# Kernel tuning notes

Hardware: AMD Instinct MI355X
Metric: run time of the kernel (lower is better)

## Reference

```python
import jax, jax.numpy as jnp
import numpy as np

N, DIN, DOUT = 8192, 512, 256


def setup_inputs() -> dict:
    key = jax.random.key(0)
    ks = jax.random.split(key, 8)
    s_in = 1.0 / np.sqrt(DIN)   # ~ torch Linear default init scale
    s_out = 1.0 / np.sqrt(DOUT)
    return {
        "x": jax.random.normal(ks[0], (N, DIN), jnp.float32),
        "Wm": jax.random.normal(ks[1], (DIN, DOUT), jnp.float32) * s_in,
        "Wn": jax.random.normal(ks[2], (DIN, DOUT), jnp.float32) * s_in,
        "Wr": jax.random.normal(ks[3], (DIN, DOUT), jnp.float32) * s_in,
        "Wt": jax.random.normal(ks[4], (DIN, DOUT), jnp.float32) * s_in,
        "Wrg": jax.random.normal(ks[5], (DOUT, DOUT), jnp.float32) * s_out,
        "brg": jnp.zeros((DOUT,), jnp.float32),
        "Wlg": jax.random.normal(ks[6], (DOUT, DOUT), jnp.float32) * s_out,
        "blg": jnp.zeros((DOUT,), jnp.float32),
        "Wp": jax.random.normal(ks[7], (DOUT, 1), jnp.float32) * s_out,
        "bp": jnp.zeros((1,), jnp.float32),
    }


def reference(x, Wm, Wn, Wr, Wt, Wrg, brg, Wlg, blg, Wp, bp):
    n = x.shape[0]
    xm = x @ Wm                      # [N, 256]
    xn = x @ Wn                      # [N, 256]
    # pairwise Euclidean distance via GEMM trick (avoids O(N^2*D) diff tensor)
    sq = (jnp.sum(xm * xm, axis=-1)[:, None]
          + jnp.sum(xn * xn, axis=-1)[None, :]
          - 2.0 * (xm @ xn.T))       # [N, N]
    dist = jnp.sqrt(jnp.maximum(sq, 0.0)) * 0.5
    exps = jnp.exp(-dist) / (n / 64.0)
    eye = jnp.eye(n, dtype=x.dtype)
    adj = exps * (1.0 - eye) + eye   # unit diagonal, scaled off-diagonal
    xr = adj @ (x @ Wr)              # graph conv: [N,N]@[N,256]
    xl = x @ Wt
    w = jax.nn.sigmoid(xr @ Wrg + brg + xl @ Wlg + blg)
    feat = (1.0 - w) * xr + w * xl   # gated fusion
    score = feat @ Wp + bp           # [N, 1]
    return adj, score
```

## Files before the change

kernel.cpp:

```cpp
#include <hip/hip_runtime.h>
#include <stdint.h>

typedef __attribute__((ext_vector_type(8))) short bf16x8;
typedef __attribute__((ext_vector_type(4))) float f32x4;
typedef __attribute__((ext_vector_type(4))) unsigned int u32x4;

__device__ __forceinline__ unsigned short f2bf(float f){
  unsigned u = __float_as_uint(f);
  u += 0x7FFFu + ((u >> 16) & 1u);
  return (unsigned short)(u >> 16);
}
__device__ __forceinline__ float bf2f(unsigned short s){
  return __uint_as_float(((unsigned)s) << 16);
}

__device__ __forceinline__ int lds_off(int r, int b){
  return r * 128 + (b ^ ((r & 7) << 4));
}
__device__ __forceinline__ int ldsP_off(int r, int b){
  return r * 256 + (b ^ ((r & 7) << 4));
}

__device__ __forceinline__ void cp16(const unsigned short* g, unsigned short* l){
  __builtin_amdgcn_global_load_lds(
      (const __attribute__((address_space(1))) unsigned int*)g,
      (__attribute__((address_space(3))) unsigned int*)l, 16, 0, 0);
}

template<int ROWS, int NT>
__device__ __forceinline__ void stage_async(unsigned short* lds, const unsigned short* g,
                                            long row0, long stride, long k0, int tid){
#pragma unroll
  for (int c = tid; c < ROWS * 8; c += NT){
    int r = c >> 3, s = c & 7;
    int ss = s ^ (r & 7);
    cp16(g + (row0 + r) * stride + k0 + ss * 8, lds + (long)(c & ~63) * 8);
  }
}

__device__ __forceinline__ int xcd_swz(int bid, int nwg){
  int q = nwg >> 3;
  return (bid & 7) * q + (bid >> 3);
}

__global__ __launch_bounds__(256) void k_prep(const float* x, const float* Wm, const float* Wn,
    const float* Wr, const float* Wt, const float* Wrg, const float* Wlg, const float* bp,
    unsigned short* WT, unsigned short* WcatT, unsigned short* xbf, float* nm, float* nn,
    float* score){
  long id = (long)blockIdx.x * 256 + threadIdx.x;
  if (id < 1024L * 512){
    int n = (int)(id >> 9), k = (int)(id & 511);
    const float* W = (n < 256) ? Wm : ((n < 512) ? Wn : ((n < 768) ? Wr : Wt));
    WT[id] = f2bf(W[(long)k * 256 + (n & 255)]);
  }
  if (id < 256L * 512){
    int n = (int)(id >> 9), k = (int)(id & 511);
    WcatT[id] = f2bf(k < 256 ? Wrg[(long)k * 256 + n] : Wlg[(long)(k - 256) * 256 + n]);
  }
  if (id < 8192){ score[id] = bp[0]; nm[id] = 0.f; nn[id] = 0.f; }
  long xe = id * 8;
  float4 v0 = *(const float4*)(x + xe);
  float4 v1 = *(const float4*)(x + xe + 4);
  unsigned short t[8] = { f2bf(v0.x), f2bf(v0.y), f2bf(v0.z), f2bf(v0.w),
                          f2bf(v1.x), f2bf(v1.y), f2bf(v1.z), f2bf(v1.w) };
  *(uint4*)(xbf + xe) = *(const uint4*)t;
}

__global__ __launch_bounds__(256, 3) void k_gemmA(const unsigned short* xbf, const unsigned short* WT,
    unsigned short* xm, unsigned short* xn, unsigned short* xwrT, unsigned short* xl,
    float* nm, float* nn){
  __shared__ unsigned short ldsA[128 * 64];
  __shared__ unsigned short ldsB[128 * 64];
  int tid = threadIdx.x, lane = tid & 63, w = tid >> 6;
  int r = lane & 15, gq = lane >> 4;
  int wi = w >> 1, wc = w & 1;
  int swz = xcd_swz(blockIdx.x, 512);
  int bm = swz & 63, bn = swz >> 6;

  f32x4 acc[4][4];
  f32x4 zero = {0.f, 0.f, 0.f, 0.f};
#pragma unroll
  for (int m = 0; m < 4; ++m)
#pragma unroll
    for (int n = 0; n < 4; ++n) acc[m][n] = zero;

  for (int k0 = 0; k0 < 512; k0 += 64){
    __syncthreads();
    stage_async<128, 256>(ldsA, xbf, (long)bm * 128, 512, k0, tid);
    stage_async<128, 256>(ldsB, WT, (long)bn * 128, 512, k0, tid);
    __syncthreads();
#pragma unroll
    for (int ks = 0; ks < 2; ++ks){
      int bb = ks * 64 + gq * 16;
      bf16x8 a[4], b[4];
#pragma unroll
      for (int m = 0; m < 4; ++m)
        a[m] = *(const bf16x8*)((const char*)ldsA + lds_off(wi * 64 + m * 16 + r, bb));
#pragma unroll
      for (int n = 0; n < 4; ++n)
        b[n] = *(const bf16x8*)((const char*)ldsB + lds_off(wc * 64 + n * 16 + r, bb));
#pragma unroll
      for (int m = 0; m < 4; ++m)
#pragma unroll
        for (int n = 0; n < 4; ++n)
          acc[m][n] = __builtin_amdgcn_mfma_f32_16x16x32_bf16(b[n], a[m], acc[m][n], 0, 0, 0);
    }
  }
#pragma unroll
  for (int m = 0; m < 4; ++m){
    int i = bm * 128 + wi * 64 + m * 16 + r;
#pragma unroll
    for (int n = 0; n < 4; ++n){
      int ng = bn * 128 + wc * 64 + n * 16 + gq * 4;
      int sector = ng >> 8, nc = ng & 255;
      unsigned short p[4] = { f2bf(acc[m][n][0]), f2bf(acc[m][n][1]),
                              f2bf(acc[m][n][2]), f2bf(acc[m][n][3]) };
      if (sector == 2){
#pragma unroll
        for (int q = 0; q < 4; ++q) xwrT[(long)(nc + q) * 8192 + i] = p[q];
      } else {
        unsigned short* dst = sector == 0 ? xm : (sector == 1 ? xn : xl);
        *(uint2*)(dst + (long)i * 256 + nc) = *(const uint2*)p;
      }
    }
    if (bn < 4){
      float s = 0.f;
#pragma unroll
      for (int n = 0; n < 4; ++n)
#pragma unroll
        for (int q = 0; q < 4; ++q) s += acc[m][n][q] * acc[m][n][q];
      s += __shfl_xor(s, 16);
      s += __shfl_xor(s, 32);
      if (gq == 0) atomicAdd(((bn < 2) ? nm : nn) + i, s);
    }
  }
}

__global__ __launch_bounds__(512, 1) void k_fused(
    const unsigned short* xm, const unsigned short* xn,
    const float* nm, const float* nn, const unsigned short* xwrT,
    float* adj, float* partial, int ntiles, int NS){
  __shared__ char smem[131072];
  char* ldsP = smem + 65536;
  unsigned short* ldsW = (unsigned short*)(smem + 98304);

  int tid = threadIdx.x, lane = tid & 63, w = tid >> 6;
  int r = lane & 15, gq = lane >> 4;
  int wi = w >> 2, wj = w & 3;
  int sp = blockIdx.x % NS, bm = blockIdx.x / NS;

  f32x4 zero = {0.f, 0.f, 0.f, 0.f};
  f32x4 acc2[4][4];
#pragma unroll
  for (int m = 0; m < 4; ++m)
#pragma unroll
    for (int n = 0; n < 4; ++n) acc2[m][n] = zero;

  float nmi[4];
#pragma unroll
  for (int m = 0; m < 4; ++m) nmi[m] = nm[bm * 128 + wi * 64 + m * 16 + r];

  long prevColBase = 0;

  for (int t = 0; t < ntiles; ++t){
    int bn = sp * ntiles + t;
    f32x4 acc1[4][2];
#pragma unroll
    for (int m = 0; m < 4; ++m)
#pragma unroll
      for (int n = 0; n < 2; ++n) acc1[m][n] = zero;

    stage_async<128, 512>((unsigned short*)smem, xm, (long)bm * 128, 256, 0, tid);
    stage_async<128, 512>((unsigned short*)(smem + 16384), xn, (long)bn * 128, 256, 0, tid);
    __syncthreads();
#pragma unroll
    for (int kk = 0; kk < 4; ++kk){
      char* cb = smem + (kk & 1) * 32768;
      if (kk < 3){
        char* nb = smem + ((kk + 1) & 1) * 32768;
        stage_async<128, 512>((unsigned short*)nb, xm, (long)bm * 128, 256, (kk + 1) * 64, tid);
        stage_async<128, 512>((unsigned short*)(nb + 16384), xn, (long)bn * 128, 256, (kk + 1) * 64, tid);
      }
      if (t > 0){
        int row = kk * 32 + (tid >> 4), cs = tid & 15;
        uint4 pv = *(const uint4*)(ldsP + ldsP_off(row, cs * 16));
        const unsigned short* pb = (const unsigned short*)&pv;
        long ge = (long)(bm * 128 + row) * 8192 + prevColBase + cs * 8;
        f32x4 v0 = { bf2f(pb[0]), bf2f(pb[1]), bf2f(pb[2]), bf2f(pb[3]) };
        f32x4 v1 = { bf2f(pb[4]), bf2f(pb[5]), bf2f(pb[6]), bf2f(pb[7]) };
        __builtin_nontemporal_store(v0, (f32x4*)(adj + ge));
        __builtin_nontemporal_store(v1, (f32x4*)(adj + ge + 4));
      }
      unsigned short* ldsA = (unsigned short*)cb;
      unsigned short* ldsB = (unsigned short*)(cb + 16384);
      __builtin_amdgcn_s_setprio(1);
#pragma unroll
      for (int ks = 0; ks < 2; ++ks){
        int bb = ks * 64 + gq * 16;
        bf16x8 a[4], b[2];
#pragma unroll
        for (int m = 0; m < 4; ++m)
          a[m] = *(const bf16x8*)((const char*)ldsA + lds_off(wi * 64 + m * 16 + r, bb));
#pragma unroll
        for (int n = 0; n < 2; ++n)
          b[n] = *(const bf16x8*)((const char*)ldsB + lds_off(wj * 32 + n * 16 + r, bb));
#pragma unroll
        for (int m = 0; m < 4; ++m)
#pragma unroll
          for (int n = 0; n < 2; ++n)
            acc1[m][n] = __builtin_amdgcn_mfma_f32_16x16x32_bf16(b[n], a[m], acc1[m][n], 0, 0, 0);
      }
      __builtin_amdgcn_s_setprio(0);
      __syncthreads();
    }

#pragma unroll
    for (int n = 0; n < 2; ++n){
      int jl0 = wj * 32 + n * 16 + gq * 4;
      int jb = bn * 128 + jl0;
      float4 nn4 = *(const float4*)(nn + jb);
      const float nnq[4] = { nn4.x, nn4.y, nn4.z, nn4.w };
#pragma unroll
      for (int m = 0; m < 4; ++m){
        int il = wi * 64 + m * 16 + r;
        int i = bm * 128 + il;
        unsigned short pv[4];
#pragma unroll
        for (int q = 0; q < 4; ++q){
          float sq = nmi[m] + nnq[q] - 2.f * acc1[m][n][q];
          float d = sqrtf(fmaxf(sq, 0.f)) * 0.5f;
          float v = (i == jb + q) ? 1.f : __expf(-d) * (1.f / 128.f);
          pv[q] = f2bf(v);
        }
        *(uint2*)(ldsP + ldsP_off(il, jl0 * 2)) = *(const uint2*)pv;
      }
    }
    __syncthreads();

#pragma unroll
    for (int kh = 0; kh < 2; ++kh){
      stage_async<256, 512>(ldsW, xwrT, 0, 8192, (long)bn * 128 + kh * 64, tid);
      __syncthreads();
      __builtin_amdgcn_s_setprio(1);
#pragma unroll
      for (int ks = 0; ks < 2; ++ks){
        bf16x8 a[4], b[4];
#pragma unroll
        for (int m = 0; m < 4; ++m)
          a[m] = *(const bf16x8*)(ldsP + ldsP_off(wi * 64 + m * 16 + r, kh * 128 + ks * 64 + gq * 16));
#pragma unroll
        for (int n = 0; n < 4; ++n)
          b[n] = *(const bf16x8*)((const char*)ldsW + lds_off(wj * 64 + n * 16 + r, ks * 64 + gq * 16));
#pragma unroll
        for (int m = 0; m < 4; ++m)
#pragma unroll
          for (int n = 0; n < 4; ++n)
            acc2[m][n] = __builtin_amdgcn_mfma_f32_16x16x32_bf16(b[n], a[m], acc2[m][n], 0, 0, 0);
      }
      __builtin_amdgcn_s_setprio(0);
      __syncthreads();
    }
    prevColBase = (long)bn * 128;
  }

#pragma unroll
  for (int o = 0; o < 4; ++o){
    int c = o * 512 + tid;
    int row = c >> 4, cs = c & 15;
    uint4 pv = *(const uint4*)(ldsP + ldsP_off(row, cs * 16));
    const unsigned short* pb = (const unsigned short*)&pv;
    long ge = (long)(bm * 128 + row) * 8192 + prevColBase + cs * 8;
    f32x4 v0 = { bf2f(pb[0]), bf2f(pb[1]), bf2f(pb[2]), bf2f(pb[3]) };
    f32x4 v1 = { bf2f(pb[4]), bf2f(pb[5]), bf2f(pb[6]), bf2f(pb[7]) };
    __builtin_nontemporal_store(v0, (f32x4*)(adj + ge));
    __builtin_nontemporal_store(v1, (f32x4*)(adj + ge + 4));
  }

  float* dst = partial + (long)sp * 8192 * 256;
#pragma unroll
  for (int m = 0; m < 4; ++m){
    int i = bm * 128 + wi * 64 + m * 16 + r;
#pragma unroll
    for (int n = 0; n < 4; ++n){
      int cb = wj * 64 + n * 16 + gq * 4;
      __builtin_nontemporal_store(acc2[m][n], (f32x4*)(dst + (long)i * 256 + cb));
    }
  }
}

__global__ __launch_bounds__(512, 2) void k_gate(const float* partial, int S,
    const unsigned short* xl, const unsigned short* WcatT,
    const float* brg, const float* blg, const float* Wp, float* score){
  __shared__ unsigned short ldsA[128 * 64];
  __shared__ unsigned short ldsB[256 * 64];
  int tid = threadIdx.x, lane = tid & 63, w = tid >> 6;
  int r = lane & 15, gq = lane >> 4;
  int wi = w >> 2, wc = w & 3;
  int bm = blockIdx.x;

  f32x4 acc[4][4];
  f32x4 zero = {0.f, 0.f, 0.f, 0.f};
#pragma unroll
  for (int m = 0; m < 4; ++m)
#pragma unroll
    for (int n = 0; n < 4; ++n) acc[m][n] = zero;

  uint2 xrf[4][4], xlf[4][4];

  for (int t = 0; t < 8; ++t){
    __syncthreads();
    if (t < 4){
#pragma unroll
      for (int u = 0; u < 2; ++u){
        int c = tid + u * 512;
        int rr = c >> 3, s = c & 7;
        long gi = (long)(bm * 128 + rr) * 256 + t * 64 + s * 8;
        f32x4 a0 = __builtin_nontemporal_load((const f32x4*)(partial + gi));
        f32x4 a1 = __builtin_nontemporal_load((const f32x4*)(partial + gi + 4));
        for (int sp = 1; sp < S; ++sp){
          long go = (long)sp * 8192 * 256 + gi;
          a0 += __builtin_nontemporal_load((const f32x4*)(partial + go));
          a1 += __builtin_nontemporal_load((const f32x4*)(partial + go + 4));
        }
        unsigned short tb[8] = { f2bf(a0[0]), f2bf(a0[1]), f2bf(a0[2]), f2bf(a0[3]),
                                 f2bf(a1[0]), f2bf(a1[1]), f2bf(a1[2]), f2bf(a1[3]) };
        *(uint4*)((char*)ldsA + lds_off(rr, s * 16)) = *(const uint4*)tb;
      }
    } else {
      stage_async<128, 512>(ldsA, xl, (long)bm * 128, 256, (t - 4) * 64, tid);
    }
    stage_async<256, 512>(ldsB, WcatT, 0, 512, (long)t * 64, tid);
    __syncthreads();

    if (t == wc || t == wc + 4){
#pragma unroll
      for (int m = 0; m < 4; ++m){
        int il = wi * 64 + m * 16 + r;
#pragma unroll
        for (int n = 0; n < 4; ++n){
          uint2 v = *(const uint2*)((const char*)ldsA + lds_off(il, (n * 16 + gq * 4) * 2));
          if (t < 4) xrf[m][n] = v; else xlf[m][n] = v;
        }
      }
    }
#pragma unroll
    for (int ks = 0; ks < 2; ++ks){
      int bb = ks * 64 + gq * 16;
      bf16x8 a[4], b[4];
#pragma unroll
      for (int m = 0; m < 4; ++m)
        a[m] = *(const bf16x8*)((const char*)ldsA + lds_off(wi * 64 + m * 16 + r, bb));
#pragma unroll
      for (int n = 0; n < 4; ++n)
        b[n] = *(const bf16x8*)((const char*)ldsB + lds_off(wc * 64 + n * 16 + r, bb));
#pragma unroll
      for (int m = 0; m < 4; ++m)
#pragma unroll
        for (int n = 0; n < 4; ++n)
          acc[m][n] = __builtin_amdgcn_mfma_f32_16x16x32_bf16(b[n], a[m], acc[m][n], 0, 0, 0);
    }
  }

#pragma unroll
  for (int m = 0; m < 4; ++m){
    int i = bm * 128 + wi * 64 + m * 16 + r;
    float part = 0.f;
#pragma unroll
    for (int n = 0; n < 4; ++n){
      int cb = wc * 64 + n * 16 + gq * 4;
      float4 b4  = *(const float4*)(brg + cb);
      float4 l4  = *(const float4*)(blg + cb);
      float4 wp4 = *(const float4*)(Wp + cb);
      const unsigned short* xr4 = (const unsigned short*)&xrf[m][n];
      const unsigned short* xl4 = (const unsigned short*)&xlf[m][n];
      const float bq[4] = { b4.x, b4.y, b4.z, b4.w };
      const float lq[4] = { l4.x, l4.y, l4.z, l4.w };
      const float pq[4] = { wp4.x, wp4.y, wp4.z, wp4.w };
#pragma unroll
      for (int q = 0; q < 4; ++q){
        float arg = acc[m][n][q] + bq[q] + lq[q];
        float wv = 1.f / (1.f + __expf(-arg));
        float feat = (1.f - wv) * bf2f(xr4[q]) + wv * bf2f(xl4[q]);
        part += feat * pq[q];
      }
    }
    part += __shfl_xor(part, 16);
    part += __shfl_xor(part, 32);
    if (gq == 0) atomicAdd(score + i, part);
  }
}

extern "C" void kernel_launch(void* const* d_in, const int* in_sizes, int n_in,
                              void* d_out, int out_size, void* d_ws, size_t ws_size,
                              hipStream_t stream){
  const float* x   = (const float*)d_in[0];
  const float* Wm  = (const float*)d_in[1];
  const float* Wn  = (const float*)d_in[2];
  const float* Wr  = (const float*)d_in[3];
  const float* Wt  = (const float*)d_in[4];
  const float* Wrg = (const float*)d_in[5];
  const float* brg = (const float*)d_in[6];
  const float* Wlg = (const float*)d_in[7];
  const float* blg = (const float*)d_in[8];
  const float* Wp  = (const float*)d_in[9];
  const float* bp  = (const float*)d_in[10];

  float* adj   = (float*)d_out;
  float* score = adj + 8192L * 8192;

  char* wsb = (char*)d_ws;
  unsigned short* xm    = (unsigned short*)(wsb);
  unsigned short* xn    = (unsigned short*)(wsb + (4L  << 20));
  unsigned short* xwrT  = (unsigned short*)(wsb + (8L  << 20));
  unsigned short* xl    = (unsigned short*)(wsb + (12L << 20));
  float*          nm    = (float*)         (wsb + (20L << 20));
  float*          nn    = nm + 8192;
  unsigned short* WT    = (unsigned short*)(wsb + (21L << 20));
  unsigned short* WcatT = (unsigned short*)(wsb + (22L << 20));
  unsigned short* xbf   = (unsigned short*)(wsb + (23L << 20));
  float*          partial = (float*)(wsb + (31L << 20));

  size_t base = 31L << 20;
  int NS = 1;
  if      (ws_size >= base + 8 * (8L << 20)) NS = 8;
  else if (ws_size >= base + 4 * (8L << 20)) NS = 4;
  else if (ws_size >= base + 2 * (8L << 20)) NS = 2;

  k_prep  <<<2048, 256, 0, stream>>>(x, Wm, Wn, Wr, Wt, Wrg, Wlg, bp, WT, WcatT, xbf, nm, nn, score);
  k_gemmA <<<512, 256, 0, stream>>>(xbf, WT, xm, xn, xwrT, xl, nm, nn);
  k_fused <<<64 * NS, 512, 0, stream>>>(xm, xn, nm, nn, xwrT, adj, partial, 64 / NS, NS);
  k_gate  <<<64, 512, 0, stream>>>(partial, NS, xl, WcatT, brg, blg, Wp, score);
}
```

Baseline: 287.9 us.

## Defer adj@xwr GEMM to next tile, load xwr directly, shrink LDS for occupancy

The fused distance/adjacency kernel now runs the second GEMM (P tile times xwr) one tile late and overlaps it with the next tile's first-GEMM staging. The xwr operand is read straight from global memory into registers, with no LDS staging. The first GEMM uses a K-step of 32 with a smaller double buffer, so LDS per block drops from 128KB to 64KB and launch bounds allow more resident blocks. In exchange, the uncoalesced global reads of xwr rely on L2, the first GEMM needs more barriers, and register pressure may rise under the higher launch-bounds target.

```diff
diff --git a/kernel.cpp b/kernel.cpp
--- a/kernel.cpp
+++ b/kernel.cpp
@@ -17,6 +17,9 @@
 __device__ __forceinline__ int lds_off(int r, int b){
   return r * 128 + (b ^ ((r & 7) << 4));
 }
+__device__ __forceinline__ int lds32_off(int r, int b){
+  return r * 64 + (b ^ ((r & 3) << 4));
+}
 __device__ __forceinline__ int ldsP_off(int r, int b){
   return r * 256 + (b ^ ((r & 7) << 4));
 }
@@ -38,9 +41,11 @@
   }
 }
 
-__device__ __forceinline__ int xcd_swz(int bid, int nwg){
-  int q = nwg >> 3;
-  return (bid & 7) * q + (bid >> 3);
+__device__ __forceinline__ void stage32(unsigned short* lds, const unsigned short* g,
+                                        long row0, long stride, long k0, int tid){
+  int r = tid >> 2, s = tid & 3;
+  int ss = s ^ (r & 3);
+  cp16(g + (row0 + r) * stride + k0 + ss * 8, lds + (long)(tid & ~63) * 8);
 }
 
 __global__ __launch_bounds__(256) void k_prep(const float* x, const float* Wm, const float* Wn,
@@ -74,7 +79,8 @@
   int tid = threadIdx.x, lane = tid & 63, w = tid >> 6;
   int r = lane & 15, gq = lane >> 4;
   int wi = w >> 1, wc = w & 1;
-  int swz = xcd_swz(blockIdx.x, 512);
+  int q8 = 512 >> 3;
+  int swz = (blockIdx.x & 7) * q8 + (blockIdx.x >> 3);
   int bm = swz & 63, bn = swz >> 6;
 
   f32x4 acc[4][4];
@@ -136,13 +142,12 @@
   }
 }
 
-__global__ __launch_bounds__(512, 1) void k_fused(
+__global__ __launch_bounds__(512, 4) void k_fused(
     const unsigned short* xm, const unsigned short* xn,
     const float* nm, const float* nn, const unsigned short* xwrT,
     float* adj, float* partial, int ntiles, int NS){
-  __shared__ char smem[131072];
-  char* ldsP = smem + 65536;
-  unsigned short* ldsW = (unsigned short*)(smem + 98304);
+  __shared__ char smem[65536];
+  char* ldsP = smem + 32768;
 
   int tid = threadIdx.x, lane = tid & 63, w = tid >> 6;
   int r = lane & 15, gq = lane >> 4;
@@ -160,56 +165,78 @@
 #pragma unroll
   for (int m = 0; m < 4; ++m) nmi[m] = nm[bm * 128 + wi * 64 + m * 16 + r];
 
-  long prevColBase = 0;
+  long prevCol = 0;
 
   for (int t = 0; t < ntiles; ++t){
     int bn = sp * ntiles + t;
-    f32x4 acc1[4][2];
-#pragma unroll
-    for (int m = 0; m < 4; ++m)
-#pragma unroll
-      for (int n = 0; n < 2; ++n) acc1[m][n] = zero;
-
-    stage_async<128, 512>((unsigned short*)smem, xm, (long)bm * 128, 256, 0, tid);
-    stage_async<128, 512>((unsigned short*)(smem + 16384), xn, (long)bn * 128, 256, 0, tid);
-    __syncthreads();
-#pragma unroll
-    for (int kk = 0; kk < 4; ++kk){
-      char* cb = smem + (kk & 1) * 32768;
-      if (kk < 3){
-        char* nb = smem + ((kk + 1) & 1) * 32768;
-        stage_async<128, 512>((unsigned short*)nb, xm, (long)bm * 128, 256, (kk + 1) * 64, tid);
-        stage_async<128, 512>((unsigned short*)(nb + 16384), xn, (long)bn * 128, 256, (kk + 1) * 64, tid);
-      }
-      if (t > 0){
-        int row = kk * 32 + (tid >> 4), cs = tid & 15;
+
+    stage32((unsigned short*)smem, xm, (long)bm * 128, 256, 0, tid);
+    stage32((unsigned short*)(smem + 8192), xn, (long)bn * 128, 256, 0, tid);
+
+    if (t > 0){
+#pragma unroll
+      for (int o = 0; o < 4; ++o){
+        int c = o * 512 + tid;
+        int row = c >> 4, cs = c & 15;
         uint4 pv = *(const uint4*)(ldsP + ldsP_off(row, cs * 16));
         const unsigned short* pb = (const unsigned short*)&pv;
-        long ge = (long)(bm * 128 + row) * 8192 + prevColBase + cs * 8;
+        long ge = (long)(bm * 128 + row) * 8192 + prevCol + cs * 8;
         f32x4 v0 = { bf2f(pb[0]), bf2f(pb[1]), bf2f(pb[2]), bf2f(pb[3]) };
         f32x4 v1 = { bf2f(pb[4]), bf2f(pb[5]), bf2f(pb[6]), bf2f(pb[7]) };
         __builtin_nontemporal_store(v0, (f32x4*)(adj + ge));
         __builtin_nontemporal_store(v1, (f32x4*)(adj + ge + 4));
       }
+#pragma unroll
+      for (int ks = 0; ks < 4; ++ks){
+        bf16x8 a[4], b[4];
+#pragma unroll
+        for (int n = 0; n < 4; ++n){
+          long c = wj * 64 + n * 16 + r;
+          b[n] = *(const bf16x8*)(xwrT + c * 8192 + prevCol + ks * 32 + gq * 8);
+        }
+#pragma unroll
+        for (int m = 0; m < 4; ++m)
+          a[m] = *(const bf16x8*)(ldsP + ldsP_off(wi * 64 + m * 16 + r, ks * 64 + gq * 16));
+        __builtin_amdgcn_s_setprio(1);
+#pragma unroll
+        for (int m = 0; m < 4; ++m)
+#pragma unroll
+          for (int n = 0; n < 4; ++n)
+            acc2[m][n] = __builtin_amdgcn_mfma_f32_16x16x32_bf16(b[n], a[m], acc2[m][n], 0, 0, 0);
+        __builtin_amdgcn_s_setprio(0);
+      }
+    }
+    __syncthreads();
+
+    f32x4 acc1[4][2];
+#pragma unroll
+    for (int m = 0; m < 4; ++m)
+#pragma unroll
+      for (int n = 0; n < 2; ++n) acc1[m][n] = zero;
+
+#pragma unroll
+    for (int kk = 0; kk < 8; ++kk){
+      char* cb = smem + (kk & 1) * 16384;
+      if (kk < 7){
+        char* nb = smem + ((kk + 1) & 1) * 16384;
+        stage32((unsigned short*)nb, xm, (long)bm * 128, 256, (kk + 1) * 32, tid);
+        stage32((unsigned short*)(nb + 8192), xn, (long)bn * 128, 256, (kk + 1) * 32, tid);
+      }
       unsigned short* ldsA = (unsigned short*)cb;
-      unsigned short* ldsB = (unsigned short*)(cb + 16384);
+      unsigned short* ldsB = (unsigned short*)(cb + 8192);
+      bf16x8 a[4], b[2];
+#pragma unroll
+      for (int m = 0; m < 4; ++m)
+        a[m] = *(const bf16x8*)((const char*)ldsA + lds32_off(wi * 64 + m * 16 + r, gq * 16));
+#pragma unroll
+      for (int n = 0; n < 2; ++n)
+        b[n] = *(const bf16x8*)((const char*)ldsB + lds32_off(wj * 32 + n * 16 + r, gq * 16));
       __builtin_amdgcn_s_setprio(1);
 #pragma unroll
-      for (int ks = 0; ks < 2; ++ks){
-        int bb = ks * 64 + gq * 16;
-        bf16x8 a[4], b[2];
-#pragma unroll
-        for (int m = 0; m < 4; ++m)
-          a[m] = *(const bf16x8*)((const char*)ldsA + lds_off(wi * 64 + m * 16 + r, bb));
+      for (int m = 0; m < 4; ++m)
 #pragma unroll
         for (int n = 0; n < 2; ++n)
-          b[n] = *(const bf16x8*)((const char*)ldsB + lds_off(wj * 32 + n * 16 + r, bb));
-#pragma unroll
-        for (int m = 0; m < 4; ++m)
-#pragma unroll
-          for (int n = 0; n < 2; ++n)
-            acc1[m][n] = __builtin_amdgcn_mfma_f32_16x16x32_bf16(b[n], a[m], acc1[m][n], 0, 0, 0);
-      }
+          acc1[m][n] = __builtin_amdgcn_mfma_f32_16x16x32_bf16(b[n], a[m], acc1[m][n], 0, 0, 0);
       __builtin_amdgcn_s_setprio(0);
       __syncthreads();
     }
@@ -235,33 +262,10 @@
         *(uint2*)(ldsP + ldsP_off(il, jl0 * 2)) = *(const uint2*)pv;
       }
     }
-    __syncthreads();
-
-#pragma unroll
-    for (int kh = 0; kh < 2; ++kh){
-      stage_async<256, 512>(ldsW, xwrT, 0, 8192, (long)bn * 128 + kh * 64, tid);
-      __syncthreads();
-      __builtin_amdgcn_s_setprio(1);
-#pragma unroll
-      for (int ks = 0; ks < 2; ++ks){
-        bf16x8 a[4], b[4];
-#pragma unroll
-        for (int m = 0; m < 4; ++m)
-          a[m] = *(const bf16x8*)(ldsP + ldsP_off(wi * 64 + m * 16 + r, kh * 128 + ks * 64 + gq * 16));
-#pragma unroll
-        for (int n = 0; n < 4; ++n)
-          b[n] = *(const bf16x8*)((const char*)ldsW + lds_off(wj * 64 + n * 16 + r, ks * 64 + gq * 16));
-#pragma unroll
-        for (int m = 0; m < 4; ++m)
-#pragma unroll
-          for (int n = 0; n < 4; ++n)
-            acc2[m][n] = __builtin_amdgcn_mfma_f32_16x16x32_bf16(b[n], a[m], acc2[m][n], 0, 0, 0);
-      }
-      __builtin_amdgcn_s_setprio(0);
-      __syncthreads();
-    }
-    prevColBase = (long)bn * 128;
-  }
+    prevCol = (long)bn * 128;
+  }
+
+  __syncthreads();
 
 #pragma unroll
   for (int o = 0; o < 4; ++o){
@@ -269,11 +273,28 @@
     int row = c >> 4, cs = c & 15;
     uint4 pv = *(const uint4*)(ldsP + ldsP_off(row, cs * 16));
     const unsigned short* pb = (const unsigned short*)&pv;
-    long ge = (long)(bm * 128 + row) * 8192 + prevColBase + cs * 8;
+    long ge = (long)(bm * 128 + row) * 8192 + prevCol + cs * 8;
     f32x4 v0 = { bf2f(pb[0]), bf2f(pb[1]), bf2f(pb[2]), bf2f(pb[3]) };
     f32x4 v1 = { bf2f(pb[4]), bf2f(pb[5]), bf2f(pb[6]), bf2f(pb[7]) };
     __builtin_nontemporal_store(v0, (f32x4*)(adj + ge));
     __builtin_nontemporal_store(v1, (f32x4*)(adj + ge + 4));
+  }
+#pragma unroll
+  for (int ks = 0; ks < 4; ++ks){
+    bf16x8 a[4], b[4];
+#pragma unroll
+    for (int n = 0; n < 4; ++n){
+      long c = wj * 64 + n * 16 + r;
+      b[n] = *(const bf16x8*)(xwrT + c * 8192 + prevCol + ks * 32 + gq * 8);
+    }
+#pragma unroll
+    for (int m = 0; m < 4; ++m)
+      a[m] = *(const bf16x8*)(ldsP + ldsP_off(wi * 64 + m * 16 + r, ks * 64 + gq * 16));
+#pragma unroll
+    for (int m = 0; m < 4; ++m)
+#pragma unroll
+      for (int n = 0; n < 4; ++n)
+        acc2[m][n] = __builtin_amdgcn_mfma_f32_16x16x32_bf16(b[n], a[m], acc2[m][n], 0, 0, 0);
   }
 
   float* dst = partial + (long)sp * 8192 * 256;
```

Measured after the change: 352.7 us. +22.5%, slower.
